# Optimization experiments

Measured on AMD Instinct MI355X. Metric: run time of the kernel, lower is better.

The kernel has to match this reference:

```python
import jax, jax.numpy as jnp
import numpy as np

N_NODES = 100000
N_EDGES = 1600000
IN_DIM, HID_DIM, OUT_DIM = 128, 256, 512
BN_EPS = 1e-5


def setup_inputs() -> dict:
    key = jax.random.key(0)
    ks = jax.random.split(key, 10)
    x = jax.random.normal(ks[0], (N_NODES, IN_DIM), dtype=jnp.float32)
    edge_index = jax.random.randint(ks[1], (2, N_EDGES), 0, N_NODES, dtype=jnp.int64)
    def lin(k, o, i):
        return jax.random.normal(k, (o, i), dtype=jnp.float32) * (1.0 / np.sqrt(i))
    return {
        "x": x,
        "edge_index": edge_index,
        # SAGEConv 1: in_dim -> hidden_dim (lin_l has bias, lin_r has none)
        "W1l": lin(ks[2], HID_DIM, IN_DIM),
        "b1": jnp.zeros((HID_DIM,), dtype=jnp.float32),
        "W1r": lin(ks[3], HID_DIM, IN_DIM),
        # BatchNorm1d(hidden_dim)
        "gamma": jnp.ones((HID_DIM,), dtype=jnp.float32),
        "beta": jnp.zeros((HID_DIM,), dtype=jnp.float32),
        # SAGEConv 2: hidden_dim -> gnn_out_dim
        "W2l": lin(ks[4], OUT_DIM, HID_DIM),
        "b2": jnp.zeros((OUT_DIM,), dtype=jnp.float32),
        "W2r": lin(ks[5], OUT_DIM, HID_DIM),
    }


def _sage_max(h, src, dst, Wl, b, Wr, n_nodes):
    # gather source features, max-aggregate onto destination nodes
    agg = jax.ops.segment_max(h[src], dst, num_segments=n_nodes)  # [N, D]
    agg = jnp.where(jnp.isneginf(agg), 0.0, agg)  # PyG fills empty segments with 0
    return agg @ Wl.T + b + h @ Wr.T


def reference(x, edge_index, W1l, b1, W1r, gamma, beta, W2l, b2, W2r):
    src, dst = edge_index[0], edge_index[1]
    n = x.shape[0]
    # layer 1: SAGEConv(in_dim, hidden_dim, aggr='max')
    h = _sage_max(x, src, dst, W1l, b1, W1r, n)
    # BatchNorm1d (batch statistics), Dropout is identity in eval; no activation in 'sage' branch
    mean = jnp.mean(h, axis=0)
    var = jnp.var(h, axis=0)
    h = gamma * (h - mean) * jax.lax.rsqrt(var + BN_EPS) + beta
    # layer 2: SAGEConv(hidden_dim, gnn_out_dim, aggr='max')
    out = _sage_max(h, src, dst, W2l, b2, W2r, n)
    return out
```

## Files before the change

kernel.cpp:

```cpp
#include <hip/hip_runtime.h>
#include <hip/hip_bf16.h>
#include <stdint.h>

#define N_NODES 100000
#define N_EDGES 1600000
#define IN_DIM 128
#define HID_DIM 256
#define OUT_DIM 512
#define NBUK 391
#define BCAP 8192
#define EPB 2048

typedef __attribute__((ext_vector_type(4))) float f32x4;
typedef __attribute__((ext_vector_type(8))) short bf16x8;

__device__ __forceinline__ float bf16lo(uint32_t u){ uint32_t b = u << 16; return __builtin_bit_cast(float, b); }
__device__ __forceinline__ float bf16hi(uint32_t u){ uint32_t b = u & 0xffff0000u; return __builtin_bit_cast(float, b); }
__device__ __forceinline__ uint16_t f32_to_bf16(float f){
  uint32_t u = __builtin_bit_cast(uint32_t, f);
  uint32_t r = (u + 0x7fffu + ((u >> 16) & 1u)) >> 16;
  return (uint16_t)r;
}
__device__ __forceinline__ uint32_t pack_bf16_exact(float lo, float hi){
  return (__builtin_bit_cast(uint32_t, hi) & 0xffff0000u) | (__builtin_bit_cast(uint32_t, lo) >> 16);
}
__device__ __forceinline__ uint32_t pack_bf16_rne(float lo, float hi){
  return (uint32_t)f32_to_bf16(lo) | ((uint32_t)f32_to_bf16(hi) << 16);
}
__device__ __forceinline__ void gl2lds16(const void* g, void* l){
  __builtin_amdgcn_global_load_lds(
      (const __attribute__((address_space(1))) uint32_t*)g,
      (__attribute__((address_space(3))) uint32_t*)l, 16, 0, 0);
}

__global__ void k_pre(const float* __restrict__ x, uint16_t* __restrict__ X1x,
                      int* __restrict__ gcur, float* __restrict__ sum,
                      float* __restrict__ sumsq, const float* __restrict__ W1l,
                      const float* __restrict__ W1r, uint16_t* __restrict__ W1cat){
  const int bid = blockIdx.x, tid = threadIdx.x;
  if (bid < 12500){
    const int idx = bid * 256 + tid;
    const int n = idx >> 5, q = idx & 31;
    const float4 v = *(const float4*)(x + (long)n * 128 + q * 4);
    ushort4 o;
    o.x = f32_to_bf16(v.x); o.y = f32_to_bf16(v.y);
    o.z = f32_to_bf16(v.z); o.w = f32_to_bf16(v.w);
    *(ushort4*)(X1x + (long)n * 128 + q * 4) = o;
  } else if (bid == 12500){
    for (int i = tid; i < NBUK; i += 256) gcur[i] = i << 13;
    sum[tid] = 0.f; sumsq[tid] = 0.f;
  } else {
    const int idx = (bid - 12501) * 256 + tid;
    const int j = idx >> 8, k = idx & 255;
    float v = (k < 128) ? W1l[j * 128 + k] : W1r[j * 128 + (k - 128)];
    W1cat[idx] = f32_to_bf16(v);
  }
}

__global__ void k_bucket(const int* __restrict__ src, const int* __restrict__ dst,
                         int* __restrict__ gcur, int* __restrict__ ebuk){
  __shared__ int hist[NBUK], curs[NBUK], base[NBUK];
  const int tid = threadIdx.x;
  const int e0 = blockIdx.x * EPB;
  for (int t = tid; t < NBUK; t += 256) hist[t] = 0;
  __syncthreads();
  for (int i = 0; i < EPB; i += 256){
    int e = e0 + i + tid;
    if (e < N_EDGES) atomicAdd(&hist[dst[e] >> 8], 1);
  }
  __syncthreads();
  for (int t = tid; t < NBUK; t += 256){
    int h = hist[t];
    base[t] = h ? atomicAdd(&gcur[t], h) : 0;
    curs[t] = 0;
  }
  __syncthreads();
  for (int i = 0; i < EPB; i += 256){
    int e = e0 + i + tid;
    if (e < N_EDGES){
      int d = dst[e];
      int b = d >> 8;
      int idx = atomicAdd(&curs[b], 1);
      int pos = base[b] + idx;
      if (pos < ((b + 1) << 13))
        ebuk[pos] = ((d & 255) << 17) | src[e];
    }
  }
}

__global__ __launch_bounds__(256)
void k_fillc(const int* __restrict__ gcur, const int* __restrict__ ebuk,
             int* __restrict__ row_start, int* __restrict__ esrc){
  __shared__ int ebuf[BCAP];
  __shared__ int cnt[256];
  __shared__ int wtot[4];
  __shared__ int red[4];
  const int b = blockIdx.x, tid = threadIdx.x, lane = tid & 63, wv = tid >> 6;
  const int nodebase = b << 8;
  const int nodecnt = min(256, N_NODES - nodebase);
  int accb = 0;
  for (int t = tid; t < b; t += 256) accb += gcur[t] - (t << 13);
  #pragma unroll
  for (int d = 32; d > 0; d >>= 1) accb += __shfl_xor(accb, d);
  if (lane == 0) red[wv] = accb;
  int size_b = gcur[b] - (b << 13);
  if (size_b > BCAP) size_b = BCAP;
  cnt[tid] = 0;
  for (int i = tid; i < size_b; i += 256) ebuf[i] = ebuk[(b << 13) + i];
  __syncthreads();
  const int bs = red[0] + red[1] + red[2] + red[3];
  for (int i = tid; i < size_b; i += 256) atomicAdd(&cnt[ebuf[i] >> 17], 1);
  __syncthreads();
  const int c = cnt[tid];
  int v = c;
  #pragma unroll
  for (int d = 1; d < 64; d <<= 1){ int t = __shfl_up(v, d); if (lane >= d) v += t; }
  if (lane == 63) wtot[wv] = v;
  __syncthreads();
  if (tid < 4){
    int t = wtot[tid];
    #pragma unroll
    for (int d = 1; d < 4; d <<= 1){ int u = __shfl_up(t, d); if (tid >= d) t += u; }
    wtot[tid] = t;
  }
  __syncthreads();
  const int excl = (wv ? wtot[wv - 1] : 0) + (v - c);
  if (tid < nodecnt) row_start[nodebase + tid] = bs + excl;
  if (b == NBUK - 1 && tid == 0) row_start[N_NODES] = N_EDGES;
  cnt[tid] = excl;
  __syncthreads();
  for (int i = tid; i < size_b; i += 256){
    int p = ebuf[i];
    int pos = atomicAdd(&cnt[p >> 17], 1);
    esrc[bs + pos] = p & 0x1FFFF;
  }
}

__global__ void k_agg1(const uint32_t* __restrict__ X1x, const int* __restrict__ row_start,
                       const int* __restrict__ esrc, uint32_t* __restrict__ X1agg){
  const int wid = (blockIdx.x * 256 + threadIdx.x) >> 6;
  const int lane = threadIdx.x & 63;
  if (wid >= N_NODES) return;
  const int grp = lane >> 4, li = lane & 15;
  const int s0 = row_start[wid], s1 = row_start[wid + 1];
  float m[8];
  #pragma unroll
  for (int j = 0; j < 8; j++) m[j] = -INFINITY;

  #define ACC1(u)                                        \
    m[0] = fmaxf(m[0], bf16lo(u.x)); m[1] = fmaxf(m[1], bf16hi(u.x)); \
    m[2] = fmaxf(m[2], bf16lo(u.y)); m[3] = fmaxf(m[3], bf16hi(u.y)); \
    m[4] = fmaxf(m[4], bf16lo(u.z)); m[5] = fmaxf(m[5], bf16hi(u.z)); \
    m[6] = fmaxf(m[6], bf16lo(u.w)); m[7] = fmaxf(m[7], bf16hi(u.w));

  int e = s0 + grp;
  for (; e + 12 < s1; e += 16){
    const uint4 ua = *(const uint4*)(X1x + (long)esrc[e] * 64 + li * 4);
    const uint4 ub = *(const uint4*)(X1x + (long)esrc[e + 4] * 64 + li * 4);
    const uint4 uc = *(const uint4*)(X1x + (long)esrc[e + 8] * 64 + li * 4);
    const uint4 ud = *(const uint4*)(X1x + (long)esrc[e + 12] * 64 + li * 4);
    ACC1(ua); ACC1(ub); ACC1(uc); ACC1(ud);
  }
  for (; e < s1; e += 4){
    const uint4 u = *(const uint4*)(X1x + (long)esrc[e] * 64 + li * 4);
    ACC1(u);
  }
  #undef ACC1
  #pragma unroll
  for (int j = 0; j < 8; j++){
    m[j] = fmaxf(m[j], __shfl_xor(m[j], 16));
    m[j] = fmaxf(m[j], __shfl_xor(m[j], 32));
  }
  if (grp == 0){
    uint4 o;
    if (s1 == s0){ o.x = o.y = o.z = o.w = 0u; }
    else {
      o.x = pack_bf16_exact(m[0], m[1]);
      o.y = pack_bf16_exact(m[2], m[3]);
      o.z = pack_bf16_exact(m[4], m[5]);
      o.w = pack_bf16_exact(m[6], m[7]);
    }
    *(uint4*)(X1agg + (long)wid * 64 + li * 4) = o;
  }
}

__global__ void k_aggw2(const uint32_t* __restrict__ X2h, const int* __restrict__ row_start,
                        const int* __restrict__ esrc, const float* __restrict__ sum,
                        const float* __restrict__ sumsq, const float* __restrict__ gamma,
                        const float* __restrict__ beta, uint32_t* __restrict__ X2agg,
                        const float* __restrict__ W2l, const float* __restrict__ W2r,
                        const float* __restrict__ b2, uint16_t* __restrict__ W2cat,
                        float* __restrict__ bias2){
  __shared__ float sc_s[256], sh_s[256];
  const int bid = blockIdx.x, tid = threadIdx.x;
  {
    const float inv_n = 1.0f / (float)N_NODES;
    float mean = sum[tid] * inv_n;
    float var = sumsq[tid] * inv_n - mean * mean;
    float sc = gamma[tid] * rsqrtf(var + 1e-5f);
    sc_s[tid] = sc;
    sh_s[tid] = beta[tid] - mean * sc;
  }
  __syncthreads();

  if (bid >= 25000){
    const int wid = ((bid - 25000) * 256 + tid) >> 6;
    const int lane = tid & 63;
    float part = 0.f;
    #pragma unroll
    for (int t = 0; t < 4; t++){
      int k = t * 64 + lane;
      float wl = W2l[(long)wid * 256 + k];
      W2cat[(long)wid * 512 + k] = f32_to_bf16(wl);
      float wr = W2r[(long)wid * 256 + k];
      W2cat[(long)wid * 512 + 256 + k] = f32_to_bf16(wr * sc_s[k]);
      part += sh_s[k] * wr;
    }
    #pragma unroll
    for (int d = 32; d > 0; d >>= 1) part += __shfl_xor(part, d);
    if (lane == 0) bias2[wid] = b2[wid] + part;
    return;
  }

  const int wid = (bid * 256 + tid) >> 6;
  const int lane = tid & 63;
  const int half = lane >> 5, li = lane & 31;
  const int c0 = li * 8;
  const float4 sca = *(const float4*)(sc_s + c0);
  const float4 scb = *(const float4*)(sc_s + c0 + 4);
  const float4 sha = *(const float4*)(sh_s + c0);
  const float4 shb = *(const float4*)(sh_s + c0 + 4);
  const int s0 = row_start[wid], s1 = row_start[wid + 1];
  float m[8];
  #pragma unroll
  for (int j = 0; j < 8; j++) m[j] = -INFINITY;

  #define ACC8(u)                                                   \
    m[0] = fmaxf(m[0], fmaf(bf16lo(u.x), sca.x, sha.x));            \
    m[1] = fmaxf(m[1], fmaf(bf16hi(u.x), sca.y, sha.y));            \
    m[2] = fmaxf(m[2], fmaf(bf16lo(u.y), sca.z, sha.z));            \
    m[3] = fmaxf(m[3], fmaf(bf16hi(u.y), sca.w, sha.w));            \
    m[4] = fmaxf(m[4], fmaf(bf16lo(u.z), scb.x, shb.x));            \
    m[5] = fmaxf(m[5], fmaf(bf16hi(u.z), scb.y, shb.y));            \
    m[6] = fmaxf(m[6], fmaf(bf16lo(u.w), scb.z, shb.z));            \
    m[7] = fmaxf(m[7], fmaf(bf16hi(u.w), scb.w, shb.w));

  int e = s0 + half;
  for (; e + 6 < s1; e += 8){
    const uint4 ua = *(const uint4*)(X2h + (long)esrc[e] * 128 + li * 4);
    const uint4 ub = *(const uint4*)(X2h + (long)esrc[e + 2] * 128 + li * 4);
    const uint4 uc = *(const uint4*)(X2h + (long)esrc[e + 4] * 128 + li * 4);
    const uint4 ud = *(const uint4*)(X2h + (long)esrc[e + 6] * 128 + li * 4);
    ACC8(ua); ACC8(ub); ACC8(uc); ACC8(ud);
  }
  for (; e < s1; e += 2){
    const uint4 u = *(const uint4*)(X2h + (long)esrc[e] * 128 + li * 4);
    ACC8(u);
  }
  #undef ACC8
  #pragma unroll
  for (int j = 0; j < 8; j++) m[j] = fmaxf(m[j], __shfl_xor(m[j], 32));
  if (half == 0){
    uint4 o;
    if (s1 == s0){ o.x = 0u; o.y = 0u; o.z = 0u; o.w = 0u; }
    else {
      o.x = pack_bf16_rne(m[0], m[1]);
      o.y = pack_bf16_rne(m[2], m[3]);
      o.z = pack_bf16_rne(m[4], m[5]);
      o.w = pack_bf16_rne(m[6], m[7]);
    }
    *(uint4*)(X2agg + (long)wid * 128 + li * 4) = o;
  }
}

template<int KT, bool EPI1>
__global__ __launch_bounds__(256, 4)
void k_gemm(const uint16_t* __restrict__ Alo, const uint16_t* __restrict__ Ahi,
            const uint16_t* __restrict__ B, const float* __restrict__ bias,
            uint16_t* __restrict__ outb, float* __restrict__ outf,
            float* __restrict__ sum, float* __restrict__ sumsq)
{
  constexpr int NSTEPS = KT / 64;
  constexpr int HSTEPS = NSTEPS / 2;
  constexpr int NT = EPI1 ? 256 : 512;
  constexpr int NW = NT / 128;
  constexpr int WG = 782 * NW;
  constexpr int PER = (WG + 7) / 8;
  __shared__ uint8_t lds[32768];
  const int bid = blockIdx.x;
  const int wgid = (bid & 7) * PER + (bid >> 3);
  if (wgid >= WG) return;
  const int mblk = wgid / NW, nblk = wgid % NW;
  const int tid = threadIdx.x, lane = tid & 63, wv = tid >> 6;
  const int wvm = wv >> 1, wvn = wv & 1;

  f32x4 acc[4][4] = {};

  const int srow = wv * 32 + (lane >> 3);
  const int skb  = (lane & 7) * 16;

  const uint8_t* asrc_lo[4];
  const uint8_t* asrc_hi[4];
  const uint8_t* bsrc[4];
  #pragma unroll
  for (int i = 0; i < 4; i++){
    int row = srow + i * 8;
    int kbsw = skb ^ ((row & 7) << 4);
    long grow = (long)mblk * 128 + row;
    if (grow > N_NODES - 1) grow = N_NODES - 1;
    asrc_lo[i] = (const uint8_t*)Alo + grow * KT + kbsw;
    asrc_hi[i] = (const uint8_t*)Ahi + grow * KT + kbsw;
    bsrc[i] = (const uint8_t*)B + ((long)nblk * 128 + row) * (KT * 2) + kbsw;
  }

  #define STAGE(ks)                                                          \
    _Pragma("unroll")                                                        \
    for (int i = 0; i < 4; i++)                                              \
      gl2lds16((ks) < HSTEPS ? asrc_lo[i] + (long)(ks) * 128                 \
                             : asrc_hi[i] + (long)((ks) - HSTEPS) * 128,     \
               &lds[(wv * 4 + i) * 1024]);                                   \
    _Pragma("unroll")                                                        \
    for (int i = 0; i < 4; i++)                                              \
      gl2lds16(bsrc[i] + (long)(ks) * 128,                                   \
               &lds[16384 + (wv * 4 + i) * 1024]);

  #pragma unroll
  for (int ks = 0; ks < NSTEPS; ++ks){
    if (ks) __syncthreads();
    STAGE(ks);
    __syncthreads();

    const uint8_t* ldsA = &lds[0];
    const uint8_t* ldsB = &lds[16384];
    #pragma unroll
    for (int kk = 0; kk < 2; kk++){
      const int kb = kk * 64 + (lane >> 4) * 16;
      bf16x8 af[4], bfr[4];
      #pragma unroll
      for (int m = 0; m < 4; m++){
        int row = wvm * 64 + m * 16 + (lane & 15);
        af[m] = *(const bf16x8*)(ldsA + row * 128 + (kb ^ ((row & 7) << 4)));
      }
      #pragma unroll
      for (int n = 0; n < 4; n++){
        int row = wvn * 64 + n * 16 + (lane & 15);
        bfr[n] = *(const bf16x8*)(ldsB + row * 128 + (kb ^ ((row & 7) << 4)));
      }
      #pragma unroll
      for (int m = 0; m < 4; m++)
        #pragma unroll
        for (int n = 0; n < 4; n++)
          acc[m][n] = __builtin_amdgcn_mfma_f32_16x16x32_bf16(af[m], bfr[n], acc[m][n], 0, 0, 0);
    }
  }
  #undef STAGE

  const int rgrp = (lane >> 4) * 4;
  #pragma unroll
  for (int n = 0; n < 4; n++){
    const int col = nblk * 128 + wvn * 64 + n * 16 + (lane & 15);
    const float bv = bias[col];
    float s1v = 0.f, s2v = 0.f;
    #pragma unroll
    for (int m = 0; m < 4; m++){
      const int rowb = mblk * 128 + wvm * 64 + m * 16 + rgrp;
      f32x4 v = acc[m][n];
      #pragma unroll
      for (int j = 0; j < 4; j++){
        const int row = rowb + j;
        const float h = v[j] + bv;
        if (row < N_NODES){
          if (EPI1){
            outb[(long)row * NT + col] = f32_to_bf16(h);
            s1v += h; s2v += h * h;
          } else {
            __builtin_nontemporal_store(h, &outf[(long)row * NT + col]);
          }
        }
      }
    }
    if (EPI1){
      s1v += __shfl_xor(s1v, 16); s1v += __shfl_xor(s1v, 32);
      s2v += __shfl_xor(s2v, 16); s2v += __shfl_xor(s2v, 32);
      if (lane < 16){
        atomicAdd(&sum[col], s1v);
        atomicAdd(&sumsq[col], s2v);
      }
    }
  }
}

extern "C" void kernel_launch(void* const* d_in, const int* in_sizes, int n_in,
                              void* d_out, int out_size, void* d_ws, size_t ws_size,
                              hipStream_t stream){
  const float* x     = (const float*)d_in[0];
  const int*   ei    = (const int*)d_in[1];
  const float* W1l   = (const float*)d_in[2];
  const float* b1    = (const float*)d_in[3];
  const float* W1r   = (const float*)d_in[4];
  const float* gamma = (const float*)d_in[5];
  const float* beta  = (const float*)d_in[6];
  const float* W2l   = (const float*)d_in[7];
  const float* b2    = (const float*)d_in[8];
  const float* W2r   = (const float*)d_in[9];
  const int* esrc_in = ei;
  const int* edst_in = ei + N_EDGES;

  uint8_t* ws = (uint8_t*)d_ws;
  uint16_t* X1agg    = (uint16_t*)(ws + 0);
  uint16_t* X1x      = (uint16_t*)(ws + 25600000);
  uint16_t* X2agg    = (uint16_t*)(ws + 51200000);
  uint16_t* X2h      = (uint16_t*)(ws + 102400000);
  int* ebuk          = (int*)(ws + 51200000);
  int* esrc          = (int*)(ws + 153600000);
  int* row_start     = (int*)(ws + 160000000);
  int* gcur          = (int*)(ws + 160402176);
  uint16_t* W1cat    = (uint16_t*)(ws + 160800256);
  uint16_t* W2cat    = (uint16_t*)(ws + 160931328);
  float* bias2       = (float*)(ws + 161455616);
  float* sum         = (float*)(ws + 161457664);
  float* sumsq       = (float*)(ws + 161458688);

  hipLaunchKernelGGL(k_pre, dim3(12757), dim3(256), 0, stream,
                     x, X1x, gcur, sum, sumsq, W1l, W1r, W1cat);
  hipLaunchKernelGGL(k_bucket, dim3(N_EDGES / EPB + 1), dim3(256), 0, stream,
                     esrc_in, edst_in, gcur, ebuk);
  hipLaunchKernelGGL(k_fillc, dim3(NBUK), dim3(256), 0, stream,
                     gcur, ebuk, row_start, esrc);
  hipLaunchKernelGGL(k_agg1, dim3(25000), dim3(256), 0, stream,
                     (const uint32_t*)X1x, row_start, esrc, (uint32_t*)X1agg);

  hipLaunchKernelGGL((k_gemm<256, true>), dim3(1568), dim3(256), 0, stream,
                     X1agg, X1x, W1cat, b1, X2h, (float*)nullptr, sum, sumsq);

  hipLaunchKernelGGL(k_aggw2, dim3(25128), dim3(256), 0, stream,
                     (const uint32_t*)X2h, row_start, esrc, sum, sumsq, gamma, beta,
                     (uint32_t*)X2agg, W2l, W2r, b2, W2cat, bias2);

  hipLaunchKernelGGL((k_gemm<512, false>), dim3(3128), dim3(256), 0, stream,
                     X2agg, X2h, W2cat, bias2, (uint16_t*)nullptr, (float*)d_out,
                     (float*)nullptr, (float*)nullptr);
}
```

Measured before the change: 389.7 us.

## Retile GEMM to 256-row M tiles with 8 waves and K-step 32

```diff
diff --git a/kernel.cpp b/kernel.cpp
--- a/kernel.cpp
+++ b/kernel.cpp
@@ -274,19 +274,20 @@
 }
 
 template<int KT, bool EPI1>
-__global__ __launch_bounds__(256, 4)
+__global__ __launch_bounds__(512, 4)
 void k_gemm(const uint16_t* __restrict__ Alo, const uint16_t* __restrict__ Ahi,
             const uint16_t* __restrict__ B, const float* __restrict__ bias,
             uint16_t* __restrict__ outb, float* __restrict__ outf,
             float* __restrict__ sum, float* __restrict__ sumsq)
 {
-  constexpr int NSTEPS = KT / 64;
+  constexpr int NSTEPS = KT / 32;
   constexpr int HSTEPS = NSTEPS / 2;
   constexpr int NT = EPI1 ? 256 : 512;
   constexpr int NW = NT / 128;
-  constexpr int WG = 782 * NW;
+  constexpr int MT = 391;
+  constexpr int WG = MT * NW;
   constexpr int PER = (WG + 7) / 8;
-  __shared__ uint8_t lds[32768];
+  __shared__ uint8_t lds[24576];
   const int bid = blockIdx.x;
   const int wgid = (bid & 7) * PER + (bid >> 3);
   if (wgid >= WG) return;
@@ -296,33 +297,30 @@
 
   f32x4 acc[4][4] = {};
 
-  const int srow = wv * 32 + (lane >> 3);
-  const int skb  = (lane & 7) * 16;
-
-  const uint8_t* asrc_lo[4];
-  const uint8_t* asrc_hi[4];
-  const uint8_t* bsrc[4];
-  #pragma unroll
-  for (int i = 0; i < 4; i++){
-    int row = srow + i * 8;
-    int kbsw = skb ^ ((row & 7) << 4);
-    long grow = (long)mblk * 128 + row;
+  const int rsub = lane >> 2;
+  const int kbs = ((lane & 3) * 16) ^ ((rsub & 3) << 4);
+
+  const uint8_t* a_lo[2];
+  const uint8_t* a_hi[2];
+  const uint8_t* b_src;
+  #pragma unroll
+  for (int j = 0; j < 2; j++){
+    long grow = (long)mblk * 256 + (wv * 2 + j) * 16 + rsub;
     if (grow > N_NODES - 1) grow = N_NODES - 1;
-    asrc_lo[i] = (const uint8_t*)Alo + grow * KT + kbsw;
-    asrc_hi[i] = (const uint8_t*)Ahi + grow * KT + kbsw;
-    bsrc[i] = (const uint8_t*)B + ((long)nblk * 128 + row) * (KT * 2) + kbsw;
-  }
+    a_lo[j] = (const uint8_t*)Alo + grow * KT + kbs;
+    a_hi[j] = (const uint8_t*)Ahi + grow * KT + kbs;
+  }
+  b_src = (const uint8_t*)B + ((long)nblk * 128 + wv * 16 + rsub) * (KT * 2) + kbs;
 
   #define STAGE(ks)                                                          \
-    _Pragma("unroll")                                                        \
-    for (int i = 0; i < 4; i++)                                              \
-      gl2lds16((ks) < HSTEPS ? asrc_lo[i] + (long)(ks) * 128                 \
-                             : asrc_hi[i] + (long)((ks) - HSTEPS) * 128,     \
-               &lds[(wv * 4 + i) * 1024]);                                   \
-    _Pragma("unroll")                                                        \
-    for (int i = 0; i < 4; i++)                                              \
-      gl2lds16(bsrc[i] + (long)(ks) * 128,                                   \
-               &lds[16384 + (wv * 4 + i) * 1024]);
+    {                                                                        \
+      const bool lo_ = (ks) < HSTEPS;                                        \
+      const long ao_ = (lo_ ? (long)(ks) : (long)((ks) - HSTEPS)) * 64;      \
+      _Pragma("unroll")                                                      \
+      for (int j = 0; j < 2; j++)                                            \
+        gl2lds16((lo_ ? a_lo[j] : a_hi[j]) + ao_, &lds[(wv * 2 + j) * 1024]);\
+      gl2lds16(b_src + (long)(ks) * 64, &lds[16384 + wv * 1024]);            \
+    }
 
   #pragma unroll
   for (int ks = 0; ks < NSTEPS; ++ks){
@@ -332,26 +330,23 @@
 
     const uint8_t* ldsA = &lds[0];
     const uint8_t* ldsB = &lds[16384];
-    #pragma unroll
-    for (int kk = 0; kk < 2; kk++){
-      const int kb = kk * 64 + (lane >> 4) * 16;
-      bf16x8 af[4], bfr[4];
+    const int kb = (lane >> 4) * 16;
+    bf16x8 af[4], bfr[4];
+    #pragma unroll
+    for (int m = 0; m < 4; m++){
+      int row = wvm * 64 + m * 16 + (lane & 15);
+      af[m] = *(const bf16x8*)(ldsA + row * 64 + (kb ^ ((row & 3) << 4)));
+    }
+    #pragma unroll
+    for (int n = 0; n < 4; n++){
+      int row = wvn * 64 + n * 16 + (lane & 15);
+      bfr[n] = *(const bf16x8*)(ldsB + row * 64 + (kb ^ ((row & 3) << 4)));
+    }
+    #pragma unroll
+    for (int m = 0; m < 4; m++)
       #pragma unroll
-      for (int m = 0; m < 4; m++){
-        int row = wvm * 64 + m * 16 + (lane & 15);
-        af[m] = *(const bf16x8*)(ldsA + row * 128 + (kb ^ ((row & 7) << 4)));
-      }
-      #pragma unroll
-      for (int n = 0; n < 4; n++){
-        int row = wvn * 64 + n * 16 + (lane & 15);
-        bfr[n] = *(const bf16x8*)(ldsB + row * 128 + (kb ^ ((row & 7) << 4)));
-      }
-      #pragma unroll
-      for (int m = 0; m < 4; m++)
-        #pragma unroll
-        for (int n = 0; n < 4; n++)
-          acc[m][n] = __builtin_amdgcn_mfma_f32_16x16x32_bf16(af[m], bfr[n], acc[m][n], 0, 0, 0);
-    }
+      for (int n = 0; n < 4; n++)
+        acc[m][n] = __builtin_amdgcn_mfma_f32_16x16x32_bf16(af[m], bfr[n], acc[m][n], 0, 0, 0);
   }
   #undef STAGE
 
@@ -363,7 +358,7 @@
     float s1v = 0.f, s2v = 0.f;
     #pragma unroll
     for (int m = 0; m < 4; m++){
-      const int rowb = mblk * 128 + wvm * 64 + m * 16 + rgrp;
+      const int rowb = mblk * 256 + wvm * 64 + m * 16 + rgrp;
       f32x4 v = acc[m][n];
       #pragma unroll
       for (int j = 0; j < 4; j++){
@@ -430,14 +425,14 @@
   hipLaunchKernelGGL(k_agg1, dim3(25000), dim3(256), 0, stream,
                      (const uint32_t*)X1x, row_start, esrc, (uint32_t*)X1agg);
 
-  hipLaunchKernelGGL((k_gemm<256, true>), dim3(1568), dim3(256), 0, stream,
+  hipLaunchKernelGGL((k_gemm<256, true>), dim3(784), dim3(512), 0, stream,
                      X1agg, X1x, W1cat, b1, X2h, (float*)nullptr, sum, sumsq);
 
   hipLaunchKernelGGL(k_aggw2, dim3(25128), dim3(256), 0, stream,
                      (const uint32_t*)X2h, row_start, esrc, sum, sumsq, gamma, beta,
                      (uint32_t*)X2agg, W2l, W2r, b2, W2cat, bias2);
 
-  hipLaunchKernelGGL((k_gemm<512, false>), dim3(3128), dim3(256), 0, stream,
+  hipLaunchKernelGGL((k_gemm<512, false>), dim3(1568), dim3(512), 0, stream,
                      X2agg, X2h, W2cat, bias2, (uint16_t*)nullptr, (float*)d_out,
                      (float*)nullptr, (float*)nullptr);
 }
```

Measured after the change: 412.9 us. 6.0% more time.
